# Performance work log

Hardware: AMD Instinct MI355X
Metric: run time of the kernel (lower is better)

The kernel has to match this reference:

```python
import jax, jax.numpy as jnp
import numpy as np

NUM_BATCHES = 2


def _bn(x, gamma, beta, eps=1e-5):
    # training-mode BatchNorm1d over active-voxel rows (biased variance, as torch)
    mu = x.mean(axis=0)
    var = x.var(axis=0)
    return (x - mu) * jax.lax.rsqrt(var + eps) * gamma + beta


def setup_inputs() -> dict:
    rng = np.random.default_rng(0)
    B, Z, Y, X = 2, 8, 512, 512
    Cin, Cout, R = 64, 128, 16
    Yo, Xo = Y // 2, X // 2
    N = 200_000
    lin = np.sort(rng.choice(B * Z * Y * X, size=N, replace=False))
    b = lin // (Z * Y * X); r = lin % (Z * Y * X)
    z = r // (Y * X); r = r % (Y * X)
    y = r // X; x = r % X
    bz = b * Z + z
    # spconv rulebook for kernel (1,3,3), stride (1,2,2), pad (0,1,1)
    in_lists, out_lists = [], []
    for ky in range(3):
        for kx in range(3):
            oy2 = y + 1 - ky; ox2 = x + 1 - kx
            ok = ((oy2 >= 0) & (oy2 % 2 == 0) & (oy2 // 2 < Yo)
                  & (ox2 >= 0) & (ox2 % 2 == 0) & (ox2 // 2 < Xo))
            idx = np.nonzero(ok)[0]
            out_lin = (bz[idx] * Yo + oy2[idx] // 2) * Xo + ox2[idx] // 2
            in_lists.append(idx); out_lists.append(out_lin)
    all_out = np.concatenate(out_lists)
    uniq, inv = np.unique(all_out, return_inverse=True)
    M = uniq.shape[0]
    P = max(len(a) for a in in_lists)
    conv_in = np.full((9, P), N, dtype=np.int32)   # pad -> zero feature row
    conv_out = np.full((9, P), M, dtype=np.int32)  # pad -> dropped garbage row
    off = 0
    for k in range(9):
        L = len(in_lists[k])
        conv_in[k, :L] = in_lists[k]
        conv_out[k, :L] = inv[off:off + L]
        off += L
    # skip: kernel 1, stride (1,2,2) -> inputs with even (y,x); its output coords
    # are always present in the main conv output set (center tap ky=kx=1)
    skip_in = np.nonzero((y % 2 == 0) & (x % 2 == 0))[0].astype(np.int32)
    skip_lin = (bz[skip_in] * Yo + y[skip_in] // 2) * Xo + x[skip_in] // 2
    skip_out = np.searchsorted(uniq, skip_lin).astype(np.int32)
    batch_of_out = (uniq // (Z * Yo * Xo)).astype(np.int32)

    key = jax.random.key(0)
    ks = jax.random.split(key, 5)
    return dict(
        features=jax.random.normal(ks[0], (N, Cin), jnp.float32),
        W_conv=jax.random.normal(ks[1], (9, Cin, Cout), jnp.float32) / np.sqrt(9 * Cin),
        W_skip=jax.random.normal(ks[2], (Cin, Cout), jnp.float32) / np.sqrt(Cin),
        bn_gamma=jnp.ones((Cout,), jnp.float32), bn_beta=jnp.zeros((Cout,), jnp.float32),
        skip_bn_gamma=jnp.ones((Cout,), jnp.float32), skip_bn_beta=jnp.zeros((Cout,), jnp.float32),
        fc1=jax.random.normal(ks[3], (Cout, Cout // R), jnp.float32) / np.sqrt(Cout),
        fc2=jax.random.normal(ks[4], (Cout // R, Cout), jnp.float32) / np.sqrt(Cout // R),
        conv_in_idx=jnp.asarray(conv_in), conv_out_idx=jnp.asarray(conv_out),
        skip_in_idx=jnp.asarray(skip_in), skip_out_idx=jnp.asarray(skip_out),
        batch_of_out=jnp.asarray(batch_of_out))


def reference(features, W_conv, W_skip, bn_gamma, bn_beta, skip_bn_gamma,
              skip_bn_beta, fc1, fc2, conv_in_idx, conv_out_idx,
              skip_in_idx, skip_out_idx, batch_of_out):
    N, Cin = features.shape
    K, _, Cout = W_conv.shape
    M = batch_of_out.shape[0]
    feats_pad = jnp.concatenate([features, jnp.zeros((1, Cin), features.dtype)], 0)
    # sparse stride-2 conv: per-offset gather -> GEMM -> scatter-add
    out = jnp.zeros((M + 1, Cout), features.dtype)
    for k in range(K):  # 9 fixed kernel taps
        contrib = feats_pad[conv_in_idx[k]] @ W_conv[k]  # [P, Cout]
        out = out.at[conv_out_idx[k]].add(contrib)
    out = _bn(out[:M], bn_gamma, bn_beta)
    # 1x1 stride-2 skip branch, BN over its own active rows, scatter to out coords
    skip_feats = _bn(features[skip_in_idx] @ W_skip, skip_bn_gamma, skip_bn_beta)
    identity = jnp.zeros((M, Cout), features.dtype).at[skip_out_idx].set(skip_feats)
    # SparseGDSCA: per-batch global-avg descriptor -> SE channel attention
    sums = jax.ops.segment_sum(out, batch_of_out, num_segments=NUM_BATCHES)
    cnts = jax.ops.segment_sum(jnp.ones((M,), out.dtype), batch_of_out, num_segments=NUM_BATCHES)
    desc = sums / cnts[:, None]                              # [B, Cout]
    attn = jax.nn.sigmoid(jax.nn.relu(desc @ fc1) @ fc2)     # [B, Cout]
    out = out * attn[batch_of_out]
    return jax.nn.relu(out + identity)                        # [M, Cout]
```

## Files before the change

### kernel.cpp

```cpp
#include <hip/hip_runtime.h>

#define CIN 64
#define COUT 128
#define NC 64
#define NSB 32
#define LDT 132
#define SKB 256
#define SB 256

typedef __bf16 bf16x8 __attribute__((ext_vector_type(8)));
typedef __bf16 bf16x4 __attribute__((ext_vector_type(4)));
typedef float  f32x4  __attribute__((ext_vector_type(4)));

__global__ __launch_bounds__(256) void prep_kernel(
    const float* __restrict__ feats, __bf16* __restrict__ fb,
    const float* __restrict__ Wc, const float* __restrict__ Ws, __bf16* __restrict__ wf,
    const int* __restrict__ cin_idx, const int* __restrict__ cout_idx, int* __restrict__ tap_in,
    const int* __restrict__ sout, int* __restrict__ inv,
    const int* __restrict__ boo, int* __restrict__ msplit,
    int total8, int P, int cpb, int Ls, int N, int M,
    int nbA, int nbAB, int nbABC, int nbABCD)
{
    const int bid = blockIdx.x, t = threadIdx.x;
    if (bid < nbA) {
        const int i = bid * 256 + t;
        if (i >= total8) return;
        const int i8 = i * 8;
        const float4 x0 = *(const float4*)(feats + i8);
        const float4 x1 = *(const float4*)(feats + i8 + 4);
        bf16x8 v;
        v[0] = (__bf16)x0.x; v[1] = (__bf16)x0.y; v[2] = (__bf16)x0.z; v[3] = (__bf16)x0.w;
        v[4] = (__bf16)x1.x; v[5] = (__bf16)x1.y; v[6] = (__bf16)x1.z; v[7] = (__bf16)x1.w;
        *(bf16x8*)(fb + i8) = v;
    } else if (bid < nbAB) {
        const int id = (bid - nbA) * 256 + t;
        if (id >= 160 * 64) return;
        const int f = id >> 6, lane = id & 63;
        const float* W; int r;
        if (f < 144) { W = Wc + (size_t)(f >> 4) * CIN * COUT; r = f & 15; }
        else         { W = Ws;                                  r = f - 144; }
        const int c = r >> 1, s = r & 1;
        const int kbase = s * 32 + (lane >> 4) * 8;
        const int col = c * 16 + (lane & 15);
        bf16x8 v;
#pragma unroll
        for (int j = 0; j < 8; ++j) v[j] = (__bf16)W[(size_t)(kbase + j) * COUT + col];
        *(bf16x8*)(wf + ((size_t)f * 64 + lane) * 8) = v;
    } else if (bid < nbABC) {
        const int c = bid - nbAB;
        const int k = c / cpb;
        const int e = (c - k * cpb) * 256 + t;
        if (e >= P) return;
        const int oo = cout_idx[(size_t)k * P + e];
        if (oo < M) tap_in[(size_t)k * M + oo] = cin_idx[(size_t)k * P + e];
    } else if (bid < nbABCD) {
        const int i = (bid - nbABC) * 256 + t;
        if (i < Ls) inv[sout[i]] = i;
    } else {
        if (t < 64) fb[(size_t)N * CIN + t] = (__bf16)0.f;
        if (t == 0) {
            int lo = 0, hi = M;
            while (lo < hi) { const int mid = (lo + hi) >> 1; if (boo[mid] < 1) lo = mid + 1; else hi = mid; }
            msplit[0] = lo;
        }
    }
}

__global__ __launch_bounds__(256) void pat_kernel(
    const int* __restrict__ tap_in, int* __restrict__ pat_arr,
    int* __restrict__ bh, int M, int N, int rpb)
{
    __shared__ int lh[512];
    const int t = threadIdx.x, bid = blockIdx.x;
    lh[t] = 0; lh[t + 256] = 0;
    __syncthreads();
    const int mend = min((bid + 1) * rpb, M);
    for (int m = bid * rpb + t; m < mend; m += 256) {
        int p = 0;
#pragma unroll
        for (int k = 0; k < 9; ++k)
            p |= (tap_in[(size_t)k * M + m] < N) << k;
        pat_arr[m] = p;
        atomicAdd(&lh[p], 1);
    }
    __syncthreads();
    bh[bid * 512 + t]       = lh[t];
    bh[bid * 512 + t + 256] = lh[t + 256];
}

__global__ __launch_bounds__(512) void scan_kernel(
    int* __restrict__ bh, int* __restrict__ ng_dev)
{
    __shared__ int buf[512];
    const int p = threadIdx.x;
    int total = 0;
    for (int b = 0; b < SB; ++b) total += bh[b * 512 + p];
    const int pc = (total + 15) & ~15;
    buf[p] = pc;
    __syncthreads();
    for (int off = 1; off < 512; off <<= 1) {
        const int v = (p >= off) ? buf[p - off] : 0;
        __syncthreads();
        buf[p] += v;
        __syncthreads();
    }
    int running = buf[p] - pc;
    if (p == 511) ng_dev[0] = buf[511] >> 4;
    for (int b = 0; b < SB; ++b) {
        const int c = bh[b * 512 + p];
        bh[b * 512 + p] = running;
        running += c;
    }
}

__global__ __launch_bounds__(256) void scatter_kernel(
    const int* __restrict__ pat_arr, const int* __restrict__ bh,
    int* __restrict__ rowid, int* __restrict__ spat, int* __restrict__ boob,
    const int* __restrict__ boo, int M, int rpb)
{
    __shared__ int lcur[512];
    const int t = threadIdx.x, bid = blockIdx.x;
    lcur[t]       = bh[bid * 512 + t];
    lcur[t + 256] = bh[bid * 512 + t + 256];
    __syncthreads();
    const int mend = min((bid + 1) * rpb, M);
    for (int m = bid * rpb + t; m < mend; m += 256) {
        const int p = pat_arr[m];
        const int pos = atomicAdd(&lcur[p], 1);
        rowid[pos] = m;
        spat[pos] = p;
        boob[pos] = boo[m];
    }
}

__global__ __launch_bounds__(256, 4) void conv_mfma_kernel(
    const __bf16* __restrict__ fb,
    const __bf16* __restrict__ wf,
    const int* __restrict__ tap_in,
    const int* __restrict__ rowid,
    const int* __restrict__ spat,
    const int* __restrict__ boob,
    const int* __restrict__ ng_dev,
    const int* __restrict__ sin_idx,
    __bf16* __restrict__ raw,
    float* __restrict__ G,
    float* __restrict__ zstats,
    int N, int M, int Ls)
{
    __shared__ float tile[4 * 16 * LDT];
    __shared__ float wred[3][4][128];
    const int t = threadIdx.x, lane = t & 63, wv = t >> 6;
    const int arow = lane & 15, apart = lane >> 4;

    if (blockIdx.x < SKB) {
        const __bf16* wk = wf + ((size_t)144 * 64 + lane) * 8;
        const bf16x8 b00 = *(const bf16x8*)(wk + (size_t)(wv * 4 + 0) * 512);
        const bf16x8 b01 = *(const bf16x8*)(wk + (size_t)(wv * 4 + 1) * 512);
        const bf16x8 b10 = *(const bf16x8*)(wk + (size_t)(wv * 4 + 2) * 512);
        const bf16x8 b11 = *(const bf16x8*)(wk + (size_t)(wv * 4 + 3) * 512);
        const int colA = wv * 32 + arow;
        const int colB = colA + 16;

        float s1A = 0.f, s2A = 0.f, s1B = 0.f, s2B = 0.f;
        const int ngroups = (Ls + 15) >> 4;
        for (int g = blockIdx.x; g < ngroups; g += SKB) {
            const int e0 = g * 16;
            const int ea = e0 + arow;
            const int ii = (ea < Ls) ? sin_idx[ea] : 0;
            const __bf16* fr = fb + (size_t)ii * CIN + apart * 8;
            const bf16x8 a0 = *(const bf16x8*)fr;
            const bf16x8 a1 = *(const bf16x8*)(fr + 32);

            f32x4 dA = {0.f,0.f,0.f,0.f};
            f32x4 dB = {0.f,0.f,0.f,0.f};
            dA = __builtin_amdgcn_mfma_f32_16x16x32_bf16(a0, b00, dA, 0, 0, 0);
            dA = __builtin_amdgcn_mfma_f32_16x16x32_bf16(a1, b01, dA, 0, 0, 0);
            dB = __builtin_amdgcn_mfma_f32_16x16x32_bf16(a0, b10, dB, 0, 0, 0);
            dB = __builtin_amdgcn_mfma_f32_16x16x32_bf16(a1, b11, dB, 0, 0, 0);

            const int er = e0 + apart * 4;
#pragma unroll
            for (int j = 0; j < 4; ++j) {
                if (er + j < Ls) {
                    const float vA = dA[j], vB = dB[j];
                    G[(size_t)(er + j) * COUT + colA] = vA;
                    G[(size_t)(er + j) * COUT + colB] = vB;
                    s1A += vA; s2A += vA * vA;
                    s1B += vB; s2B += vB * vB;
                }
            }
        }
        s1A += __shfl_xor(s1A, 16); s1A += __shfl_xor(s1A, 32);
        s2A += __shfl_xor(s2A, 16); s2A += __shfl_xor(s2A, 32);
        s1B += __shfl_xor(s1B, 16); s1B += __shfl_xor(s1B, 32);
        s2B += __shfl_xor(s2B, 16); s2B += __shfl_xor(s2B, 32);
        if (apart == 0) {
            wred[0][0][colA] = s1A; wred[0][0][colB] = s1B;
            wred[1][0][colA] = s2A; wred[1][0][colB] = s2B;
        }
        __syncthreads();
        float* bucket = zstats + NC * 384 + (size_t)(blockIdx.x & (NSB - 1)) * 256;
        if (t < 128) {
            atomicAdd(&bucket[t],       wred[0][0][t]);
            atomicAdd(&bucket[128 + t], wred[1][0][t]);
        }
        return;
    }

    const int ng = ng_dev[0];
    const int g = (blockIdx.x - SKB) * 4 + wv;
    const bool live = g < ng;
    const int m0 = g * 16;

    f32x4 D[8];
#pragma unroll
    for (int c = 0; c < 8; ++c) D[c] = (f32x4){0.f,0.f,0.f,0.f};

    int rid = -1, pattern = 0;
    if (live) {
        rid = rowid[m0 + arow];
        pattern = spat[m0];
    }

    for (int pk = pattern; pk; pk &= (pk - 1)) {
        const int k = __builtin_ctz(pk);
        const int vi = (rid >= 0) ? tap_in[(size_t)k * M + rid] : N;
        const __bf16* f0 = fb + (size_t)vi * CIN + apart * 8;
        const bf16x8 a0 = *(const bf16x8*)f0;
        const bf16x8 a1 = *(const bf16x8*)(f0 + 32);
        const __bf16* wb = wf + ((size_t)(k * 16) * 64 + lane) * 8;
#pragma unroll
        for (int c = 0; c < 8; ++c) {
            const bf16x8 b0 = *(const bf16x8*)(wb + (size_t)(c * 2 + 0) * 512);
            const bf16x8 b1 = *(const bf16x8*)(wb + (size_t)(c * 2 + 1) * 512);
            D[c] = __builtin_amdgcn_mfma_f32_16x16x32_bf16(a0, b0, D[c], 0, 0, 0);
            D[c] = __builtin_amdgcn_mfma_f32_16x16x32_bf16(a1, b1, D[c], 0, 0, 0);
        }
    }

    float ssum[8], sq[8], s0[8];
#pragma unroll
    for (int c = 0; c < 8; ++c) { ssum[c] = 0.f; sq[c] = 0.f; s0[c] = 0.f; }
    int4 bb = {1, 1, 1, 1};
    if (live) bb = *(const int4*)&boob[m0 + apart * 4];
#pragma unroll
    for (int c = 0; c < 8; ++c) {
        const float v0 = D[c][0], v1 = D[c][1], v2 = D[c][2], v3 = D[c][3];
        ssum[c] += v0 + v1 + v2 + v3;
        sq[c]   += v0*v0 + v1*v1 + v2*v2 + v3*v3;
        if (bb.x == 0) s0[c] += v0;
        if (bb.y == 0) s0[c] += v1;
        if (bb.z == 0) s0[c] += v2;
        if (bb.w == 0) s0[c] += v3;
    }

    float* T = tile + wv * (16 * LDT);
#pragma unroll
    for (int c = 0; c < 8; ++c)
#pragma unroll
        for (int j = 0; j < 4; ++j)
            T[(apart * 4 + j) * LDT + c * 16 + arow] = D[c][j];
    if (live) {
#pragma unroll
        for (int i = 0; i < 8; ++i) {
            const int r = i * 2 + (lane >> 5);
            const int c4 = (lane & 31) * 4;
            const f32x4 vv = *(const f32x4*)&T[r * LDT + c4];
            bf16x4 o;
            o[0] = (__bf16)vv[0]; o[1] = (__bf16)vv[1];
            o[2] = (__bf16)vv[2]; o[3] = (__bf16)vv[3];
            *(bf16x4*)&raw[(size_t)(m0 + r) * 128 + c4] = o;
        }
    }

#pragma unroll
    for (int c = 0; c < 8; ++c) {
        ssum[c] += __shfl_xor(ssum[c], 16); ssum[c] += __shfl_xor(ssum[c], 32);
        s0[c]   += __shfl_xor(s0[c], 16);   s0[c]   += __shfl_xor(s0[c], 32);
        sq[c]   += __shfl_xor(sq[c], 16);   sq[c]   += __shfl_xor(sq[c], 32);
    }
    if (apart == 0) {
#pragma unroll
        for (int c = 0; c < 8; ++c) {
            const int col = c * 16 + arow;
            wred[0][wv][col] = s0[c];
            wred[1][wv][col] = ssum[c] - s0[c];
            wred[2][wv][col] = sq[c];
        }
    }
    __syncthreads();
    float* bucket = zstats + (size_t)(blockIdx.x & (NC - 1)) * 384;
    if (t < 128) {
        atomicAdd(&bucket[t],       wred[0][0][t] + wred[0][1][t] + wred[0][2][t] + wred[0][3][t]);
        atomicAdd(&bucket[128 + t], wred[1][0][t] + wred[1][1][t] + wred[1][2][t] + wred[1][3][t]);
        atomicAdd(&bucket[256 + t], wred[2][0][t] + wred[2][1][t] + wred[2][2][t] + wred[2][3][t]);
    }
}

__global__ __launch_bounds__(128) void params_kernel(
    const float* __restrict__ zstats,
    const int* __restrict__ msplit_p,
    const float* __restrict__ gamma, const float* __restrict__ beta,
    const float* __restrict__ sgamma, const float* __restrict__ sbeta,
    const float* __restrict__ fc1, const float* __restrict__ fc2,
    float* __restrict__ scale, float* __restrict__ shift,
    float* __restrict__ sscale, float* __restrict__ sshift,
    float* __restrict__ attn,
    int Ls, int M)
{
    __shared__ float desc[2][COUT];
    __shared__ float hid[2][8];
    const int ch = threadIdx.x;

    float s0 = 0.f, s1 = 0.f, q = 0.f;
    for (int b = 0; b < NC; ++b) {
        const float* st = zstats + (size_t)b * 384;
        s0 += st[ch]; s1 += st[128 + ch]; q += st[256 + ch];
    }
    float ss = 0.f, sqk = 0.f;
    const float* sk = zstats + NC * 384;
    for (int b = 0; b < NSB; ++b) {
        ss  += sk[(size_t)b * 256 + ch];
        sqk += sk[(size_t)b * 256 + 128 + ch];
    }

    const float c0 = (float)msplit_p[0], c1 = (float)M - c0;
    const float Mf = (float)M;
    const float mu  = (s0 + s1) / Mf;
    const float var = q / Mf - mu * mu;
    const float rs  = rsqrtf(var + 1e-5f);
    const float sc  = rs * gamma[ch];
    const float sh  = beta[ch] - mu * sc;
    scale[ch] = sc;
    shift[ch] = sh;
    desc[0][ch] = (s0 / c0) * sc + sh;
    desc[1][ch] = (s1 / c1) * sc + sh;

    const float lsf  = (float)Ls;
    const float mus  = ss / lsf;
    const float vars = sqk / lsf - mus * mus;
    const float rss  = rsqrtf(vars + 1e-5f);
    const float ssc  = rss * sgamma[ch];
    sscale[ch] = ssc;
    sshift[ch] = sbeta[ch] - mus * ssc;

    __syncthreads();
    if (ch < 16) {
        const int b = ch >> 3, h = ch & 7;
        float a = 0.f;
        for (int c = 0; c < COUT; ++c) a += desc[b][c] * fc1[c * 8 + h];
        hid[b][h] = fmaxf(a, 0.f);
    }
    __syncthreads();
    for (int b = 0; b < 2; ++b) {
        float a = 0.f;
        for (int h = 0; h < 8; ++h) a += hid[b][h] * fc2[h * COUT + ch];
        attn[b * COUT + ch] = 1.f / (1.f + expf(-a));
    }
}

__global__ __launch_bounds__(256) void final_kernel(
    const __bf16* __restrict__ raw,
    const int* __restrict__ rowid,
    const int* __restrict__ boob,
    float* __restrict__ out,
    const float* __restrict__ G,
    const int* __restrict__ inv_skip,
    const float* __restrict__ scale, const float* __restrict__ shift,
    const float* __restrict__ sscale, const float* __restrict__ sshift,
    const float* __restrict__ attn,
    int Smax)
{
    const int t  = threadIdx.x;
    const int c4 = (t & 31) * 4;
    const int rw = t >> 5;
    const float4 sc  = *(const float4*)&scale[c4];
    const float4 sh  = *(const float4*)&shift[c4];
    const float4 ssc = *(const float4*)&sscale[c4];
    const float4 ssh = *(const float4*)&sshift[c4];
    const float4 at0 = *(const float4*)&attn[c4];
    const float4 at1 = *(const float4*)&attn[COUT + c4];

    for (int s = blockIdx.x * 8 + rw; s < Smax; s += gridDim.x * 8) {
        const int rid = rowid[s];
        if (rid < 0) continue;
        const bf16x4 rv = *(const bf16x4*)&raw[(size_t)s * COUT + c4];
        const int b = boob[s];
        const int j = inv_skip[rid];
        const float4 av = b ? at1 : at0;
        float4 y;
        y.x = ((float)rv[0] * sc.x + sh.x) * av.x;
        y.y = ((float)rv[1] * sc.y + sh.y) * av.y;
        y.z = ((float)rv[2] * sc.z + sh.z) * av.z;
        y.w = ((float)rv[3] * sc.w + sh.w) * av.w;
        if (j >= 0) {
            const float4 gg = *(const float4*)&G[(size_t)j * COUT + c4];
            y.x += gg.x * ssc.x + ssh.x;
            y.y += gg.y * ssc.y + ssh.y;
            y.z += gg.z * ssc.z + ssh.z;
            y.w += gg.w * ssc.w + ssh.w;
        }
        y.x = y.x > 0.f ? y.x : 0.f;
        y.y = y.y > 0.f ? y.y : 0.f;
        y.z = y.z > 0.f ? y.z : 0.f;
        y.w = y.w > 0.f ? y.w : 0.f;
        *(float4*)&out[(size_t)rid * COUT + c4] = y;
    }
}

extern "C" void kernel_launch(void* const* d_in, const int* in_sizes, int n_in,
                              void* d_out, int out_size, void* d_ws, size_t ws_size,
                              hipStream_t stream)
{
    const float* feats  = (const float*)d_in[0];
    const float* Wc     = (const float*)d_in[1];
    const float* Wsk    = (const float*)d_in[2];
    const float* gamma  = (const float*)d_in[3];
    const float* beta   = (const float*)d_in[4];
    const float* sgamma = (const float*)d_in[5];
    const float* sbeta  = (const float*)d_in[6];
    const float* fc1    = (const float*)d_in[7];
    const float* fc2    = (const float*)d_in[8];
    const int* cin_idx  = (const int*)d_in[9];
    const int* cout_idx = (const int*)d_in[10];
    const int* sin_idx  = (const int*)d_in[11];
    const int* sout_idx = (const int*)d_in[12];
    const int* boo      = (const int*)d_in[13];

    const int N  = in_sizes[0] / CIN;
    const int P  = in_sizes[9] / 9;
    const int Ls = in_sizes[11];
    const int M  = in_sizes[13];
    const int maxS = ((M + 15) & ~15) + 512 * 16;
    const int maxG = maxS >> 4;
    const int rpb = (M + SB - 1) / SB;

    float* out = (float*)d_out;

    char* ws = (char*)d_ws;
    __bf16* fb = (__bf16*)ws;
    size_t off = (size_t)(N + 1) * CIN * sizeof(__bf16);
    off = (off + 255) & ~(size_t)255;
    __bf16* wfrag = (__bf16*)(ws + off);
    off += (size_t)160 * 64 * 8 * sizeof(__bf16);
    off = (off + 255) & ~(size_t)255;
    int* tap_in = (int*)(ws + off);
    off += (size_t)9 * M * sizeof(int);
    off = (off + 255) & ~(size_t)255;
    float* G = (float*)(ws + off);
    off += (size_t)Ls * COUT * sizeof(float);
    int* inv_skip = (int*)(ws + off);
    off += (size_t)M * sizeof(int);
    off = (off + 255) & ~(size_t)255;
    int* pat_arr = (int*)(ws + off);
    off += (size_t)M * sizeof(int);
    off = (off + 255) & ~(size_t)255;
    int* rowid = (int*)(ws + off);
    off += (size_t)maxS * sizeof(int);
    int* spat = (int*)(ws + off);
    off += (size_t)maxS * sizeof(int);
    int* boob = (int*)(ws + off);
    off += (size_t)maxS * sizeof(int);
    off = (off + 255) & ~(size_t)255;
    __bf16* raw = (__bf16*)(ws + off);
    off += (size_t)maxS * COUT * sizeof(__bf16);
    off = (off + 255) & ~(size_t)255;
    int* bh = (int*)(ws + off);
    off += (size_t)SB * 512 * sizeof(int);
    int* ng_dev = (int*)(ws + off);
    off += 256;
    float* zstats = (float*)(ws + off);
    off += (size_t)(NC * 384 + NSB * 256) * sizeof(float);
    int* msplit = (int*)(ws + off);
    off += 256;
    float* params = (float*)(ws + off);
    float* scale = params, *shift = params + 128;
    float* sscale = params + 256, *sshift = params + 384, *attn = params + 512;

    hipMemsetAsync(zstats, 0, (size_t)(NC * 384 + NSB * 256) * sizeof(float), stream);
    hipMemsetAsync(inv_skip, 0xFF, (size_t)M * sizeof(int), stream);
    hipMemsetAsync(tap_in, 0x7F, (size_t)9 * M * sizeof(int), stream);
    hipMemsetAsync(rowid, 0xFF, (size_t)maxS * sizeof(int), stream);
    hipMemsetAsync(boob, 0, (size_t)maxS * sizeof(int), stream);

    const int total8 = N * CIN / 8;
    const int nbA = (total8 + 255) / 256;
    const int nbB = (160 * 64 + 255) / 256;
    const int cpb = (P + 255) / 256;
    const int nbAB = nbA + nbB;
    const int nbABC = nbAB + 9 * cpb;
    const int nbABCD = nbABC + (Ls + 255) / 256;
    prep_kernel<<<nbABCD + 1, 256, 0, stream>>>(
        feats, fb, Wc, Wsk, wfrag, cin_idx, cout_idx, tap_in, sout_idx, inv_skip,
        boo, msplit, total8, P, cpb, Ls, N, M, nbA, nbAB, nbABC, nbABCD);

    pat_kernel<<<SB, 256, 0, stream>>>(tap_in, pat_arr, bh, M, N, rpb);
    scan_kernel<<<1, 512, 0, stream>>>(bh, ng_dev);
    scatter_kernel<<<SB, 256, 0, stream>>>(pat_arr, bh, rowid, spat, boob, boo, M, rpb);

    conv_mfma_kernel<<<SKB + (maxG + 3) / 4, 256, 0, stream>>>(
        fb, wfrag, tap_in, rowid, spat, boob, ng_dev, sin_idx,
        raw, G, zstats, N, M, Ls);

    params_kernel<<<1, 128, 0, stream>>>(
        zstats, msplit, gamma, beta, sgamma, sbeta, fc1, fc2,
        scale, shift, sscale, sshift, attn, Ls, M);

    final_kernel<<<2048, 256, 0, stream>>>(
        raw, rowid, boob, out, G, inv_skip,
        scale, shift, sscale, sshift, attn, maxS);
}
```

Baseline: 218.1 us.

## Build tap patterns in prep, store skip GEMM as bf16, trim memsets

The per-row tap pattern is now built with atomicOr while prep fills tap_in. This drops pat_kernel's nine strided reads of tap_in. The memsets for tap_in, rowid and boob are removed: scan_kernel now marks only padding slots as -1, and final_kernel loops only up to the real padded row count. The skip-branch intermediate G is stored in bf16 rather than fp32, halving its write and read traffic. The risks are bf16 rounding of the skip values before BN, and any code that still reads tap_in or boob entries that are no longer initialised.

```diff
diff --git a/kernel.cpp b/kernel.cpp
--- a/kernel.cpp
+++ b/kernel.cpp
@@ -16,6 +16,7 @@
     const float* __restrict__ feats, __bf16* __restrict__ fb,
     const float* __restrict__ Wc, const float* __restrict__ Ws, __bf16* __restrict__ wf,
     const int* __restrict__ cin_idx, const int* __restrict__ cout_idx, int* __restrict__ tap_in,
+    int* __restrict__ pat_arr,
     const int* __restrict__ sout, int* __restrict__ inv,
     const int* __restrict__ boo, int* __restrict__ msplit,
     int total8, int P, int cpb, int Ls, int N, int M,
@@ -52,7 +53,10 @@
         const int e = (c - k * cpb) * 256 + t;
         if (e >= P) return;
         const int oo = cout_idx[(size_t)k * P + e];
-        if (oo < M) tap_in[(size_t)k * M + oo] = cin_idx[(size_t)k * P + e];
+        if (oo < M) {
+            tap_in[(size_t)k * M + oo] = cin_idx[(size_t)k * P + e];
+            atomicOr(&pat_arr[oo], 1 << k);
+        }
     } else if (bid < nbABCD) {
         const int i = (bid - nbABC) * 256 + t;
         if (i < Ls) inv[sout[i]] = i;
@@ -67,29 +71,22 @@
 }
 
 __global__ __launch_bounds__(256) void pat_kernel(
-    const int* __restrict__ tap_in, int* __restrict__ pat_arr,
-    int* __restrict__ bh, int M, int N, int rpb)
+    const int* __restrict__ pat_arr, int* __restrict__ bh, int M, int rpb)
 {
     __shared__ int lh[512];
     const int t = threadIdx.x, bid = blockIdx.x;
     lh[t] = 0; lh[t + 256] = 0;
     __syncthreads();
     const int mend = min((bid + 1) * rpb, M);
-    for (int m = bid * rpb + t; m < mend; m += 256) {
-        int p = 0;
-#pragma unroll
-        for (int k = 0; k < 9; ++k)
-            p |= (tap_in[(size_t)k * M + m] < N) << k;
-        pat_arr[m] = p;
-        atomicAdd(&lh[p], 1);
-    }
+    for (int m = bid * rpb + t; m < mend; m += 256)
+        atomicAdd(&lh[pat_arr[m]], 1);
     __syncthreads();
     bh[bid * 512 + t]       = lh[t];
     bh[bid * 512 + t + 256] = lh[t + 256];
 }
 
 __global__ __launch_bounds__(512) void scan_kernel(
-    int* __restrict__ bh, int* __restrict__ ng_dev)
+    int* __restrict__ bh, int* __restrict__ rowid, int* __restrict__ ng_dev)
 {
     __shared__ int buf[512];
     const int p = threadIdx.x;
@@ -111,6 +108,7 @@
         bh[b * 512 + p] = running;
         running += c;
     }
+    for (int x = running; x < buf[p]; ++x) rowid[x] = -1;
 }
 
 __global__ __launch_bounds__(256) void scatter_kernel(
@@ -143,7 +141,7 @@
     const int* __restrict__ ng_dev,
     const int* __restrict__ sin_idx,
     __bf16* __restrict__ raw,
-    float* __restrict__ G,
+    __bf16* __restrict__ G,
     float* __restrict__ zstats,
     int N, int M, int Ls)
 {
@@ -183,8 +181,8 @@
             for (int j = 0; j < 4; ++j) {
                 if (er + j < Ls) {
                     const float vA = dA[j], vB = dB[j];
-                    G[(size_t)(er + j) * COUT + colA] = vA;
-                    G[(size_t)(er + j) * COUT + colB] = vB;
+                    G[(size_t)(er + j) * COUT + colA] = (__bf16)vA;
+                    G[(size_t)(er + j) * COUT + colB] = (__bf16)vB;
                     s1A += vA; s2A += vA * vA;
                     s1B += vB; s2B += vB * vB;
                 }
@@ -363,13 +361,13 @@
     const __bf16* __restrict__ raw,
     const int* __restrict__ rowid,
     const int* __restrict__ boob,
+    const int* __restrict__ ng_dev,
     float* __restrict__ out,
-    const float* __restrict__ G,
+    const __bf16* __restrict__ G,
     const int* __restrict__ inv_skip,
     const float* __restrict__ scale, const float* __restrict__ shift,
     const float* __restrict__ sscale, const float* __restrict__ sshift,
-    const float* __restrict__ attn,
-    int Smax)
+    const float* __restrict__ attn)
 {
     const int t  = threadIdx.x;
     const int c4 = (t & 31) * 4;
@@ -380,8 +378,9 @@
     const float4 ssh = *(const float4*)&sshift[c4];
     const float4 at0 = *(const float4*)&attn[c4];
     const float4 at1 = *(const float4*)&attn[COUT + c4];
-
-    for (int s = blockIdx.x * 8 + rw; s < Smax; s += gridDim.x * 8) {
+    const int S = ng_dev[0] << 4;
+
+    for (int s = blockIdx.x * 8 + rw; s < S; s += gridDim.x * 8) {
         const int rid = rowid[s];
         if (rid < 0) continue;
         const bf16x4 rv = *(const bf16x4*)&raw[(size_t)s * COUT + c4];
@@ -394,11 +393,11 @@
         y.z = ((float)rv[2] * sc.z + sh.z) * av.z;
         y.w = ((float)rv[3] * sc.w + sh.w) * av.w;
         if (j >= 0) {
-            const float4 gg = *(const float4*)&G[(size_t)j * COUT + c4];
-            y.x += gg.x * ssc.x + ssh.x;
-            y.y += gg.y * ssc.y + ssh.y;
-            y.z += gg.z * ssc.z + ssh.z;
-            y.w += gg.w * ssc.w + ssh.w;
+            const bf16x4 gg = *(const bf16x4*)&G[(size_t)j * COUT + c4];
+            y.x += (float)gg[0] * ssc.x + ssh.x;
+            y.y += (float)gg[1] * ssc.y + ssh.y;
+            y.z += (float)gg[2] * ssc.z + ssh.z;
+            y.w += (float)gg[3] * ssc.w + ssh.w;
         }
         y.x = y.x > 0.f ? y.x : 0.f;
         y.y = y.y > 0.f ? y.y : 0.f;
@@ -447,8 +446,9 @@
     int* tap_in = (int*)(ws + off);
     off += (size_t)9 * M * sizeof(int);
     off = (off + 255) & ~(size_t)255;
-    float* G = (float*)(ws + off);
-    off += (size_t)Ls * COUT * sizeof(float);
+    __bf16* G = (__bf16*)(ws + off);
+    off += (size_t)Ls * COUT * sizeof(__bf16);
+    off = (off + 255) & ~(size_t)255;
     int* inv_skip = (int*)(ws + off);
     off += (size_t)M * sizeof(int);
     off = (off + 255) & ~(size_t)255;
@@ -479,9 +479,7 @@
 
     hipMemsetAsync(zstats, 0, (size_t)(NC * 384 + NSB * 256) * sizeof(float), stream);
     hipMemsetAsync(inv_skip, 0xFF, (size_t)M * sizeof(int), stream);
-    hipMemsetAsync(tap_in, 0x7F, (size_t)9 * M * sizeof(int), stream);
-    hipMemsetAsync(rowid, 0xFF, (size_t)maxS * sizeof(int), stream);
-    hipMemsetAsync(boob, 0, (size_t)maxS * sizeof(int), stream);
+    hipMemsetAsync(pat_arr, 0, (size_t)M * sizeof(int), stream);
 
     const int total8 = N * CIN / 8;
     const int nbA = (total8 + 255) / 256;
@@ -491,11 +489,12 @@
     const int nbABC = nbAB + 9 * cpb;
     const int nbABCD = nbABC + (Ls + 255) / 256;
     prep_kernel<<<nbABCD + 1, 256, 0, stream>>>(
-        feats, fb, Wc, Wsk, wfrag, cin_idx, cout_idx, tap_in, sout_idx, inv_skip,
-        boo, msplit, total8, P, cpb, Ls, N, M, nbA, nbAB, nbABC, nbABCD);
-
-    pat_kernel<<<SB, 256, 0, stream>>>(tap_in, pat_arr, bh, M, N, rpb);
-    scan_kernel<<<1, 512, 0, stream>>>(bh, ng_dev);
+        feats, fb, Wc, Wsk, wfrag, cin_idx, cout_idx, tap_in, pat_arr,
+        sout_idx, inv_skip, boo, msplit,
+        total8, P, cpb, Ls, N, M, nbA, nbAB, nbABC, nbABCD);
+
+    pat_kernel<<<SB, 256, 0, stream>>>(pat_arr, bh, M, rpb);
+    scan_kernel<<<1, 512, 0, stream>>>(bh, rowid, ng_dev);
     scatter_kernel<<<SB, 256, 0, stream>>>(pat_arr, bh, rowid, spat, boob, boo, M, rpb);
 
     conv_mfma_kernel<<<SKB + (maxG + 3) / 4, 256, 0, stream>>>(
@@ -507,6 +506,6 @@
         scale, shift, sscale, sshift, attn, Ls, M);
 
     final_kernel<<<2048, 256, 0, stream>>>(
-        raw, rowid, boob, out, G, inv_skip,
-        scale, shift, sscale, sshift, attn, maxS);
-}
+        raw, rowid, boob, ng_dev, out, G, inv_skip,
+        scale, shift, sscale, sshift, attn);
+}
```

New measurement: 212.2 us. 1.03x faster.
